# Performance work log

Measured on AMD Instinct MI355X. Metric: run time of the kernel, lower is better.

## Reference

```python
import jax, jax.numpy as jnp
import numpy as np

N, P, C, K = 16, 2048, 64, 16
EPS = 1e-5


def _bn(x, gamma, beta, axes):
    # training-mode batchnorm: biased variance over all dims except channel (last)
    m = jnp.mean(x, axis=axes, keepdims=True)
    v = jnp.var(x, axis=axes, keepdims=True)
    return (x - m) * jax.lax.rsqrt(v + EPS) * gamma + beta


def setup_inputs() -> dict:
    key = jax.random.key(0)
    ks = jax.random.split(key, 16)
    w = lambda k, shape: jax.random.normal(k, shape, jnp.float32) * 0.05
    inp = {"features": jax.random.normal(ks[0], (N, C, P), jnp.float32)}
    # edge-conv MLP: layer 0 takes 2*C input channels
    inp["w0"], inp["b0"] = w(ks[1], (C, 2 * C)), jnp.zeros((C,), jnp.float32)
    inp["g0"], inp["be0"] = jnp.ones((C,), jnp.float32), jnp.zeros((C,), jnp.float32)
    inp["w1"], inp["b1"] = w(ks[2], (C, C)), jnp.zeros((C,), jnp.float32)
    inp["g1"], inp["be1"] = jnp.ones((C,), jnp.float32), jnp.zeros((C,), jnp.float32)
    inp["w2"], inp["b2"] = w(ks[3], (C, C)), jnp.zeros((C,), jnp.float32)
    inp["g2"], inp["be2"] = jnp.ones((C,), jnp.float32), jnp.zeros((C,), jnp.float32)
    # shortcut 1x1 conv + BN
    inp["ws"], inp["bs"] = w(ks[4], (C, C)), jnp.zeros((C,), jnp.float32)
    inp["gs"], inp["bes"] = jnp.ones((C,), jnp.float32), jnp.zeros((C,), jnp.float32)
    return inp


def reference(features, w0, b0, g0, be0, w1, b1, g1, be1, w2, b2, g2, be2, ws, bs, gs, bes):
    # index != 0: features come in as (N, C, P) -> (N, P, C)
    X = jnp.transpose(features, (0, 2, 1))  # (N, P, C)

    # --- KNN via full pairwise squared distances ---
    r = jnp.sum(X * X, axis=-1)  # (N, P)
    d = r[:, :, None] - 2.0 * jnp.einsum('npc,nqc->npq', X, X) + r[:, None, :]
    _, idx = jax.lax.top_k(-d, K + 1)
    idx = idx[:, :, 1:]  # drop self, (N, P, K)

    # --- irregular gather + edge-feature concat ---
    f = X[jnp.arange(X.shape[0])[:, None, None], idx]  # (N, P, K, C)
    fc = jnp.broadcast_to(X[:, :, None, :], f.shape)   # center feature tiled
    h = jnp.concatenate([fc, fc - f], axis=-1)         # (N, P, K, 2C)

    def conv_bn_relu(h, w, b, g, be):
        h = jnp.einsum('npki,oi->npko', h, w) + b
        return jax.nn.relu(_bn(h, g, be, (0, 1, 2)))

    h = conv_bn_relu(h, w0, b0, g0, be0)
    h = conv_bn_relu(h, w1, b1, g1, be1)
    h = conv_bn_relu(h, w2, b2, g2, be2)
    h = jnp.mean(h, axis=2)  # aggregate over K -> (N, P, C)

    # shortcut: 1x1 conv + BN on center features
    sc = jnp.einsum('npi,oi->npo', X, ws) + bs
    sc = _bn(sc, gs, bes, (0, 1))

    out = jax.nn.relu(h + sc)           # (N, P, C)
    return jnp.transpose(out, (0, 2, 1))  # (N, C, P) to match torch layout
```

## Files before the change

### kernel.cpp

```cpp
#include <hip/hip_runtime.h>

using u16    = unsigned short;
using u64    = unsigned long long;
using bf16x8 = __attribute__((ext_vector_type(8))) short;
using f32x4  = __attribute__((ext_vector_type(4))) float;
using u16x4  = __attribute__((ext_vector_type(4))) u16;

#define NB   16
#define PP   2048
#define CC   64
#define KK   16
#define MROWS (NB*PP*KK)
#define NPTS  (NB*PP)

__device__ __forceinline__ float b2f(u16 u) { return __uint_as_float(((unsigned)u) << 16); }
__device__ __forceinline__ u16 f2b(float f) {
  unsigned u = __float_as_uint(f);
  return (u16)((u + 0x7fffu + ((u >> 16) & 1u)) >> 16);
}

__device__ __forceinline__ u64 dkey(float d, int qi) {
  unsigned u = __float_as_uint(d);
  u = u ^ (((unsigned)((int)u >> 31)) | 0x80000000u);
  return ((u64)u << 32) | (unsigned)qi;
}

template<bool UP>
__device__ __forceinline__ void ce(u64 &a, u64 &b) {
  const bool lt = a < b;
  const u64 lo = lt ? a : b;
  const u64 hi = lt ? b : a;
  if (UP) { a = lo; b = hi; } else { a = hi; b = lo; }
}

__device__ __forceinline__ void sort16(u64 (&v)[16]) {
  #pragma unroll
  for (int k = 2; k <= 16; k <<= 1) {
    #pragma unroll
    for (int j = k >> 1; j > 0; j >>= 1) {
      #pragma unroll
      for (int i = 0; i < 16; ++i) {
        const int l = i ^ j;
        if (l > i) {
          if ((i & k) == 0) ce<true>(v[i], v[l]);
          else              ce<false>(v[i], v[l]);
        }
      }
    }
  }
}

__device__ __forceinline__ void merge16(u64 (&dl)[16], const u64 (&nb)[16]) {
  u64 t[16];
  #pragma unroll
  for (int s = 0; s < 16; ++s) {
    const u64 a = dl[s], b = nb[15 - s];
    t[s] = a < b ? a : b;
  }
  #pragma unroll
  for (int j = 8; j > 0; j >>= 1) {
    #pragma unroll
    for (int i = 0; i < 16; ++i) {
      const int l = i ^ j;
      if (l > i) ce<true>(t[i], t[l]);
    }
  }
  #pragma unroll
  for (int s = 0; s < 16; ++s) dl[s] = t[s];
}

__global__ __launch_bounds__(256) void prep_k(const float* __restrict__ F,
                                              float* __restrict__ X,
                                              u16* __restrict__ Xb,
                                              float* __restrict__ r) {
  int gidx = blockIdx.x * 256 + threadIdx.x;
  int n = gidx >> 11, p = gidx & 2047;
  const float* src = F + (size_t)n * CC * PP + p;
  float v[CC];
  float rr = 0.f;
  #pragma unroll
  for (int c = 0; c < CC; ++c) { v[c] = src[(size_t)c * PP]; rr += v[c] * v[c]; }
  float* dst = X + (size_t)gidx * CC;
  #pragma unroll
  for (int c = 0; c < CC; c += 4) {
    float4 w; w.x = v[c]; w.y = v[c+1]; w.z = v[c+2]; w.w = v[c+3];
    *(float4*)(dst + c) = w;
  }
  u16* db = Xb + (size_t)gidx * CC;
  #pragma unroll
  for (int c = 0; c < CC; c += 8) {
    bf16x8 w8;
    #pragma unroll
    for (int j = 0; j < 8; ++j) w8[j] = (short)f2b(v[c + j]);
    *(bf16x8*)(db + c) = w8;
  }
  r[gidx] = rr;
}

__global__ __launch_bounds__(256) void cvtw_k(const float* __restrict__ w0, const float* __restrict__ w1,
                                              const float* __restrict__ w2, const float* __restrict__ wsb,
                                              u16* __restrict__ b0, u16* __restrict__ b1,
                                              u16* __restrict__ b2, u16* __restrict__ bs) {
  int i = blockIdx.x * 256 + threadIdx.x;
  if (i < 8192)        b0[i]          = f2b(w0[i]);
  else if (i < 12288)  b1[i - 8192]   = f2b(w1[i - 8192]);
  else if (i < 16384)  b2[i - 12288]  = f2b(w2[i - 12288]);
  else if (i < 20480)  bs[i - 16384]  = f2b(wsb[i - 16384]);
}

__global__ __launch_bounds__(512, 4) __attribute__((amdgpu_waves_per_eu(4, 4)))
void knn_k(const float* __restrict__ X,
           const float* __restrict__ r,
           int* __restrict__ idx) {
  __shared__ float lds[12800];
  float* Xp = lds;
  float* Xq = lds + 4352;

  const int n  = blockIdx.x >> 5;
  const int pb = (blockIdx.x & 31) * 64;
  const int t  = threadIdx.x;
  const float* Xn = X + (size_t)n * PP * CC;
  const float* rb = r + (size_t)n * PP;

  const int qh   = t & 31;
  const int pg   = t >> 5;
  const int prow = t & 63;
  const int w8   = t >> 6;
  const int u4   = (prow & 7) * 4;

  {
    const int pr = t & 63, ct = t >> 6;
    const float* src = Xn + (size_t)(pb + pr) * CC + ct * 8;
    #pragma unroll
    for (int j = 0; j < 8; j += 4) {
      float4 v = *(const float4*)(src + j);
      Xp[(ct*8 + j + 0) * 68 + pr] = v.x;
      Xp[(ct*8 + j + 1) * 68 + pr] = v.y;
      Xp[(ct*8 + j + 2) * 68 + pr] = v.z;
      Xp[(ct*8 + j + 3) * 68 + pr] = v.w;
    }
  }

  u64 dl[16];
  #pragma unroll
  for (int s = 0; s < 16; ++s) dl[s] = ~0ULL;

  #pragma unroll 1
  for (int qb = 0; qb < PP; qb += 128) {
    __syncthreads();
    {
      const int qr = t & 127, hs = t >> 7;
      const float* src = Xn + (size_t)(qb + qr) * CC + hs * 16;
      #pragma unroll
      for (int j = 0; j < 16; j += 4) {
        float4 v = *(const float4*)(src + j);
        Xq[(hs*16 + j + 0) * 132 + qr] = v.x;
        Xq[(hs*16 + j + 1) * 132 + qr] = v.y;
        Xq[(hs*16 + j + 2) * 132 + qr] = v.z;
        Xq[(hs*16 + j + 3) * 132 + qr] = v.w;
      }
    }
    __syncthreads();

    float acc[4][4];
    #pragma unroll
    for (int i = 0; i < 4; ++i)
      #pragma unroll
      for (int j = 0; j < 4; ++j) acc[i][j] = 0.f;

    #pragma unroll 4
    for (int c = 0; c < 64; ++c) {
      const float4 a = *(const float4*)&Xp[c*68 + pg*4];
      const float4 bq = *(const float4*)&Xq[c*132 + qh*4];
      float av[4] = {a.x, a.y, a.z, a.w};
      float bv[4] = {bq.x, bq.y, bq.z, bq.w};
      #pragma unroll
      for (int i = 0; i < 4; ++i)
        #pragma unroll
        for (int j = 0; j < 4; ++j)
          acc[i][j] = fmaf(av[i], bv[j], acc[i][j]);
    }
    __syncthreads();

    {
      const int qg0 = qb + qh*4;
      const float4 rv = *(const float4*)(rb + qg0);
      #pragma unroll
      for (int i = 0; i < 4; ++i) {
        const int p  = pg*4 + i;
        const int pgl = pb + p;
        float d0 = rv.x - 2.f * acc[i][0]; if (qg0 + 0 == pgl) d0 = 3.0e38f;
        float d1 = rv.y - 2.f * acc[i][1]; if (qg0 + 1 == pgl) d1 = 3.0e38f;
        float d2 = rv.z - 2.f * acc[i][2]; if (qg0 + 2 == pgl) d2 = 3.0e38f;
        float d3 = rv.w - 2.f * acc[i][3]; if (qg0 + 3 == pgl) d3 = 3.0e38f;
        float4 dv; dv.x = d0; dv.y = d1; dv.z = d2; dv.w = d3;
        *(float4*)&Xq[(size_t)p * 132 + ((qh ^ ((p & 7) * 4)) * 4)] = dv;
      }
    }
    __syncthreads();

    {
      u64 nb[16];
      const float* drow = &Xq[(size_t)prow * 132];
      const int bbase = (w8 * 4) ^ u4;
      #pragma unroll
      for (int bb = 0; bb < 4; ++bb) {
        const float4 dv = *(const float4*)(drow + (bbase + bb) * 4);
        const int qg = qb + (w8*4 + bb) * 4;
        nb[bb*4+0] = dkey(dv.x, qg+0);
        nb[bb*4+1] = dkey(dv.y, qg+1);
        nb[bb*4+2] = dkey(dv.z, qg+2);
        nb[bb*4+3] = dkey(dv.w, qg+3);
      }
      sort16(nb);
      merge16(dl, nb);
    }
  }

  __syncthreads();
  {
    u64* mb = (u64*)lds;
    if (t >= 256) {
      #pragma unroll
      for (int s = 0; s < 16; ++s) mb[s * 256 + (t - 256)] = dl[s];
    }
    __syncthreads();
    if (t < 256) {
      u64 nb[16];
      #pragma unroll
      for (int s = 0; s < 16; ++s) nb[s] = mb[s * 256 + t];
      merge16(dl, nb);
    }
    __syncthreads();
    if (t < 256) {
      #pragma unroll
      for (int s = 0; s < 16; ++s) mb[s * 256 + t] = dl[s];
    }
    __syncthreads();
    if (t < 64) {
      #pragma unroll 1
      for (int j = 1; j < 4; ++j) {
        u64 nb[16];
        #pragma unroll
        for (int s = 0; s < 16; ++s) nb[s] = mb[s * 256 + (t + 64 * j)];
        merge16(dl, nb);
      }
      #pragma unroll
      for (int s = 0; s < 16; ++s)
        idx[((size_t)n * PP + pb + t) * KK + s] = (int)(dl[s] & 0xFFFFFFFFu);
    }
  }
}

template<int KIN, bool GATHER, bool BNRELU>
__global__ __launch_bounds__(256) void conv_k(const u16* __restrict__ in,
                                              const int* __restrict__ idxp,
                                              const u16* __restrict__ wb,
                                              const float* __restrict__ bias,
                                              const float* __restrict__ st,
                                              u16* __restrict__ yout,
                                              float* __restrict__ partials) {
  constexpr int NKB = KIN / 32;
  __shared__ float sred[4][4][32];
  const int t = threadIdx.x;
  const int wv = t >> 6, l = t & 63, hi = l >> 4, lo = l & 15;
  const int rbase = blockIdx.x * 256 + wv * 64;

  bf16x8 wf[4][NKB];
  #pragma unroll
  for (int ob = 0; ob < 4; ++ob)
    #pragma unroll
    for (int kb = 0; kb < NKB; ++kb)
      wf[ob][kb] = *(const bf16x8*)(wb + (size_t)(ob*16 + lo) * KIN + kb*32 + hi*8);

  int qv[4];
  if constexpr (GATHER) {
    #pragma unroll
    for (int rb = 0; rb < 4; ++rb) {
      const int g = (rbase + rb*16) >> 4;
      qv[rb] = idxp[g * KK + lo];
    }
  }

  f32x4 acc[4][4];
  #pragma unroll
  for (int a = 0; a < 4; ++a)
    #pragma unroll
    for (int b = 0; b < 4; ++b) { f32x4 z = {0.f, 0.f, 0.f, 0.f}; acc[a][b] = z; }

  #pragma unroll
  for (int kb = 0; kb < NKB; ++kb) {
    float sv[8], tv[8];
    if constexpr (BNRELU) {
      const int k0 = kb*32 + hi*8;
      *(float4*)&sv[0] = *(const float4*)(st + k0);
      *(float4*)&sv[4] = *(const float4*)(st + k0 + 4);
      *(float4*)&tv[0] = *(const float4*)(st + KIN + k0);
      *(float4*)&tv[4] = *(const float4*)(st + KIN + k0 + 4);
    }
    bf16x8 af[4];
    #pragma unroll
    for (int rb = 0; rb < 4; ++rb) {
      if constexpr (GATHER) {
        const int g  = (rbase + rb*16) >> 4;
        const int k0 = kb*32 + hi*8;
        const bf16x8 fc = *(const bf16x8*)(in + (size_t)g * CC + (k0 & 63));
        if (kb < 2) {
          af[rb] = fc;
        } else {
          const int nn = g >> 11;
          const bf16x8 fv = *(const bf16x8*)(in + (size_t)(nn * PP + qv[rb]) * CC + (k0 & 63));
          bf16x8 df;
          #pragma unroll
          for (int j = 0; j < 8; ++j)
            df[j] = (short)f2b(b2f((u16)fc[j]) - b2f((u16)fv[j]));
          af[rb] = df;
        }
      } else {
        const int row = rbase + rb*16 + lo;
        const bf16x8 rv = *(const bf16x8*)(in + (size_t)row * KIN + kb*32 + hi*8);
        if constexpr (BNRELU) {
          bf16x8 tr;
          #pragma unroll
          for (int j = 0; j < 8; ++j) {
            const float x = fmaxf(b2f((u16)rv[j]) * sv[j] + tv[j], 0.f);
            tr[j] = (short)f2b(x);
          }
          af[rb] = tr;
        } else {
          af[rb] = rv;
        }
      }
    }
    #pragma unroll
    for (int ob = 0; ob < 4; ++ob)
      #pragma unroll
      for (int rb = 0; rb < 4; ++rb)
        acc[rb][ob] = __builtin_amdgcn_mfma_f32_16x16x32_bf16(wf[ob][kb], af[rb], acc[rb][ob], 0, 0, 0);
  }

  float ssum[16], qsum[16];
  #pragma unroll
  for (int j = 0; j < 16; ++j) { ssum[j] = 0.f; qsum[j] = 0.f; }
  #pragma unroll
  for (int ob = 0; ob < 4; ++ob) {
    const int o0 = ob*16 + hi*4;
    const float4 bv = *(const float4*)(bias + o0);
    #pragma unroll
    for (int rb = 0; rb < 4; ++rb) {
      const int row = rbase + rb*16 + lo;
      const float v0 = acc[rb][ob][0] + bv.x;
      const float v1 = acc[rb][ob][1] + bv.y;
      const float v2 = acc[rb][ob][2] + bv.z;
      const float v3 = acc[rb][ob][3] + bv.w;
      u16x4 pk; pk[0] = f2b(v0); pk[1] = f2b(v1); pk[2] = f2b(v2); pk[3] = f2b(v3);
      *(u16x4*)(yout + (size_t)row * CC + o0) = pk;
      ssum[ob*4+0] += v0; qsum[ob*4+0] += v0*v0;
      ssum[ob*4+1] += v1; qsum[ob*4+1] += v1*v1;
      ssum[ob*4+2] += v2; qsum[ob*4+2] += v2*v2;
      ssum[ob*4+3] += v3; qsum[ob*4+3] += v3*v3;
    }
  }
  #pragma unroll
  for (int m = 1; m < 16; m <<= 1) {
    #pragma unroll
    for (int j = 0; j < 16; ++j) {
      ssum[j] += __shfl_xor(ssum[j], m, 64);
      qsum[j] += __shfl_xor(qsum[j], m, 64);
    }
  }
  if (lo == 0) {
    #pragma unroll
    for (int j = 0; j < 16; ++j) {
      sred[wv][hi][j*2]   = ssum[j];
      sred[wv][hi][j*2+1] = qsum[j];
    }
  }
  __syncthreads();
  if (t < 128) {
    const int c = t & 63, half = t >> 6;
    const int slot = ((c >> 4) * 4 + (c & 3)) * 2 + half;
    const int h2 = (c >> 2) & 3;
    const float v = sred[0][h2][slot] + sred[1][h2][slot] + sred[2][h2][slot] + sred[3][h2][slot];
    partials[(size_t)blockIdx.x * 128 + half * 64 + c] = v;
  }
}

__global__ __launch_bounds__(256) void red1_k(const float* __restrict__ partials,
                                              float* __restrict__ out, int nwg) {
  __shared__ float accs[2][128];
  const int t = threadIdx.x, e = t & 127, h = t >> 7;
  float s = 0.f;
  for (int w = blockIdx.x + h * 64; w < nwg; w += 128)
    s += partials[(size_t)w * 128 + e];
  accs[h][e] = s;
  __syncthreads();
  if (t < 128) out[(size_t)blockIdx.x * 128 + t] = accs[0][t] + accs[1][t];
}

__global__ __launch_bounds__(128) void red2_k(const float* __restrict__ p2,
                                              const float* __restrict__ g,
                                              const float* __restrict__ be,
                                              float* __restrict__ st, float invM) {
  __shared__ float sq[128];
  const int t = threadIdx.x;
  float s = 0.f;
  #pragma unroll 8
  for (int w = 0; w < 64; ++w) s += p2[w * 128 + t];
  sq[t] = s;
  __syncthreads();
  if (t < 64) {
    const float S = sq[t], Q = sq[64 + t];
    const float m = S * invM;
    const float v = fmaxf(Q * invM - m * m, 0.f);
    const float sc = g[t] * rsqrtf(v + 1e-5f);
    st[t] = sc;
    st[64 + t] = be[t] - m * sc;
  }
}

__global__ __launch_bounds__(256) void final_k(const u16* __restrict__ y2,
                                               const u16* __restrict__ ysc,
                                               const float* __restrict__ st2,
                                               const float* __restrict__ stS,
                                               float* __restrict__ out) {
  __shared__ float ot[64][68];
  const int b = blockIdx.x, t = threadIdx.x;
  const int n = b >> 5, p0 = (b & 31) * 64;
  const int phh = t >> 2, jh = t & 3, c0 = jh * 16;
  const int g = n * PP + p0 + phh;
  float acc[16];
  #pragma unroll
  for (int i = 0; i < 16; ++i) acc[i] = 0.f;
  float sv[16], tv[16];
  #pragma unroll
  for (int i = 0; i < 16; ++i) { sv[i] = st2[c0 + i]; tv[i] = st2[64 + c0 + i]; }
  for (int k = 0; k < KK; ++k) {
    const u16* rp = y2 + ((size_t)g * KK + k) * CC + c0;
    const bf16x8 v0 = *(const bf16x8*)rp;
    const bf16x8 v1 = *(const bf16x8*)(rp + 8);
    #pragma unroll
    for (int j = 0; j < 8; ++j) {
      acc[j]     += fmaxf(b2f((u16)v0[j]) * sv[j]     + tv[j],     0.f);
      acc[8 + j] += fmaxf(b2f((u16)v1[j]) * sv[8 + j] + tv[8 + j], 0.f);
    }
  }
  const u16* sp = ysc + (size_t)g * CC + c0;
  const bf16x8 s0 = *(const bf16x8*)sp;
  const bf16x8 s1 = *(const bf16x8*)(sp + 8);
  #pragma unroll
  for (int i = 0; i < 16; ++i) {
    const float scx = b2f((u16)(i < 8 ? s0[i] : s1[i - 8])) * stS[c0 + i] + stS[64 + c0 + i];
    ot[c0 + i][phh] = fmaxf(acc[i] * (1.f / 16.f) + scx, 0.f);
  }
  __syncthreads();
  const int c = t >> 2, pc = t & 3;
  const float* src = &ot[c][pc * 16];
  float* dst = out + (size_t)n * CC * PP + (size_t)c * PP + p0 + pc * 16;
  #pragma unroll
  for (int j = 0; j < 16; j += 4) *(float4*)(dst + j) = *(const float4*)(src + j);
}

extern "C" void kernel_launch(void* const* d_in, const int* in_sizes, int n_in,
                              void* d_out, int out_size, void* d_ws, size_t ws_size,
                              hipStream_t stream) {
  (void)in_sizes; (void)n_in; (void)out_size; (void)ws_size;
  const float* F   = (const float*)d_in[0];
  const float* w0  = (const float*)d_in[1];
  const float* b0  = (const float*)d_in[2];
  const float* g0  = (const float*)d_in[3];
  const float* be0 = (const float*)d_in[4];
  const float* w1  = (const float*)d_in[5];
  const float* b1  = (const float*)d_in[6];
  const float* g1  = (const float*)d_in[7];
  const float* be1 = (const float*)d_in[8];
  const float* w2  = (const float*)d_in[9];
  const float* b2  = (const float*)d_in[10];
  const float* g2  = (const float*)d_in[11];
  const float* be2 = (const float*)d_in[12];
  const float* wS  = (const float*)d_in[13];
  const float* bS  = (const float*)d_in[14];
  const float* gS  = (const float*)d_in[15];
  const float* beS = (const float*)d_in[16];

  char* ws = (char*)d_ws;
  size_t off = 0;
  auto carve = [&](size_t bytes) -> void* {
    void* p = ws + off;
    off += (bytes + 255) & ~(size_t)255;
    return p;
  };
  float* X        = (float*)carve((size_t)NPTS * CC * 4);
  u16*   Xb       = (u16*)  carve((size_t)NPTS * CC * 2);
  float* rr       = (float*)carve((size_t)NPTS * 4);
  int*   idx      = (int*)  carve((size_t)NPTS * KK * 4);
  u16*   wb0      = (u16*)  carve(8192 * 2);
  u16*   wb1      = (u16*)  carve(4096 * 2);
  u16*   wb2      = (u16*)  carve(4096 * 2);
  u16*   wbs      = (u16*)  carve(4096 * 2);
  u16*   y        = (u16*)  carve((size_t)MROWS * CC * 2);
  u16*   ysc      = (u16*)  carve((size_t)NPTS * CC * 2);
  float* partials = (float*)carve((size_t)2048 * 128 * 4);
  float* p2       = (float*)carve((size_t)64 * 128 * 4);
  float* st0      = (float*)carve(128 * 4);
  float* st1      = (float*)carve(128 * 4);
  float* st2      = (float*)carve(128 * 4);
  float* stS      = (float*)carve(128 * 4);

  prep_k<<<NPTS / 256, 256, 0, stream>>>(F, X, Xb, rr);
  cvtw_k<<<80, 256, 0, stream>>>(w0, w1, w2, wS, wb0, wb1, wb2, wbs);
  knn_k<<<NB * (PP / 64), 512, 0, stream>>>(X, rr, idx);

  conv_k<128, true,  false><<<MROWS / 256, 256, 0, stream>>>(Xb, idx, wb0, b0, nullptr, y, partials);
  red1_k<<<64, 256, 0, stream>>>(partials, p2, MROWS / 256);
  red2_k<<<1, 128, 0, stream>>>(p2, g0, be0, st0, 1.f / (float)MROWS);

  conv_k<64, false, true><<<MROWS / 256, 256, 0, stream>>>(y, nullptr, wb1, b1, st0, y, partials);
  red1_k<<<64, 256, 0, stream>>>(partials, p2, MROWS / 256);
  red2_k<<<1, 128, 0, stream>>>(p2, g1, be1, st1, 1.f / (float)MROWS);

  conv_k<64, false, true><<<MROWS / 256, 256, 0, stream>>>(y, nullptr, wb2, b2, st1, y, partials);
  red1_k<<<64, 256, 0, stream>>>(partials, p2, MROWS / 256);
  red2_k<<<1, 128, 0, stream>>>(p2, g2, be2, st2, 1.f / (float)MROWS);

  conv_k<64, false, false><<<NPTS / 256, 256, 0, stream>>>(Xb, nullptr, wbs, bS, nullptr, ysc, partials);
  red1_k<<<64, 256, 0, stream>>>(partials, p2, NPTS / 256);
  red2_k<<<1, 128, 0, stream>>>(p2, gS, beS, stS, 1.f / (float)NPTS);

  final_k<<<NB * (PP / 64), 256, 0, stream>>>(y, ysc, st2, stS, (float*)d_out);
}
```

Baseline: 419.0 us.

## Split KNN query range across four blocks and merge partial top-k in new kernel

The KNN kernel now splits the 2048 query points of each batch into four 512-point chunks, launching four times as many blocks. Each block writes its partial sorted top-16 keys to a scratch buffer aliased onto the y activation buffer, and a new merge kernel combines the four partial lists into the final indices. The aim is more parallelism: the original 512 blocks of 512 threads likely underfilled the GPU. The fixed waves-per-EU attribute is also dropped. The cost is an extra kernel launch and the round trip of the partial lists through global memory.

```diff
diff --git a/kernel.cpp b/kernel.cpp
--- a/kernel.cpp
+++ b/kernel.cpp
@@ -108,16 +108,18 @@
   else if (i < 20480)  bs[i - 16384]  = f2b(wsb[i - 16384]);
 }
 
-__global__ __launch_bounds__(512, 4) __attribute__((amdgpu_waves_per_eu(4, 4)))
+__global__ __launch_bounds__(512, 4)
 void knn_k(const float* __restrict__ X,
            const float* __restrict__ r,
-           int* __restrict__ idx) {
+           u64* __restrict__ part) {
   __shared__ float lds[12800];
   float* Xp = lds;
   float* Xq = lds + 4352;
 
-  const int n  = blockIdx.x >> 5;
-  const int pb = (blockIdx.x & 31) * 64;
+  const int n  = blockIdx.x >> 7;
+  const int pb = ((blockIdx.x >> 2) & 31) * 64;
+  const int qq = blockIdx.x & 3;
+  const int qstart = qq * 512;
   const int t  = threadIdx.x;
   const float* Xn = X + (size_t)n * PP * CC;
   const float* rb = r + (size_t)n * PP;
@@ -146,7 +148,7 @@
   for (int s = 0; s < 16; ++s) dl[s] = ~0ULL;
 
   #pragma unroll 1
-  for (int qb = 0; qb < PP; qb += 128) {
+  for (int qb = qstart; qb < qstart + 512; qb += 128) {
     __syncthreads();
     {
       const int qr = t & 127, hs = t >> 7;
@@ -245,11 +247,30 @@
         for (int s = 0; s < 16; ++s) nb[s] = mb[s * 256 + (t + 64 * j)];
         merge16(dl, nb);
       }
-      #pragma unroll
-      for (int s = 0; s < 16; ++s)
-        idx[((size_t)n * PP + pb + t) * KK + s] = (int)(dl[s] & 0xFFFFFFFFu);
-    }
-  }
+      u64* outp = part + (((size_t)n * PP + pb + t) * 4 + qq) * 16;
+      #pragma unroll
+      for (int s = 0; s < 16; ++s) outp[s] = dl[s];
+    }
+  }
+}
+
+__global__ __launch_bounds__(256) void knnm_k(const u64* __restrict__ part,
+                                              int* __restrict__ idx) {
+  const int row = blockIdx.x * 256 + threadIdx.x;
+  const u64* p = part + (size_t)row * 64;
+  u64 dl[16];
+  #pragma unroll
+  for (int s = 0; s < 16; ++s) dl[s] = p[s];
+  #pragma unroll 1
+  for (int j = 1; j < 4; ++j) {
+    u64 nb[16];
+    #pragma unroll
+    for (int s = 0; s < 16; ++s) nb[s] = p[j * 16 + s];
+    merge16(dl, nb);
+  }
+  #pragma unroll
+  for (int s = 0; s < 16; ++s)
+    idx[(size_t)row * KK + s] = (int)(dl[s] & 0xFFFFFFFFu);
 }
 
 template<int KIN, bool GATHER, bool BNRELU>
@@ -507,9 +528,12 @@
   float* st2      = (float*)carve(128 * 4);
   float* stS      = (float*)carve(128 * 4);
 
+  u64* part = (u64*)y;
+
   prep_k<<<NPTS / 256, 256, 0, stream>>>(F, X, Xb, rr);
   cvtw_k<<<80, 256, 0, stream>>>(w0, w1, w2, wS, wb0, wb1, wb2, wbs);
-  knn_k<<<NB * (PP / 64), 512, 0, stream>>>(X, rr, idx);
+  knn_k<<<NB * 32 * 4, 512, 0, stream>>>(X, rr, part);
+  knnm_k<<<NPTS / 256, 256, 0, stream>>>(part, idx);
 
   conv_k<128, true,  false><<<MROWS / 256, 256, 0, stream>>>(Xb, idx, wb0, b0, nullptr, y, partials);
   red1_k<<<64, 256, 0, stream>>>(partials, p2, MROWS / 256);
```

Result: slower. 429.2 us (+2.5%).
